# Kernel tuning notes

Hardware: AMD Instinct MI355X
Metric: run time of the kernel (lower is better)

## Reference

```python
import jax, jax.numpy as jnp
import numpy as np

W_SCALE = 0.05  # keep gates out of hard saturation


def _lstm_dir(x_tbd, Wih, Whh, b, reverse):
    """One direction of one LSTM layer. x_tbd: [T,B,Din]. Returns hs [T,B,H]."""
    H = Whh.shape[1]
    B = x_tbd.shape[1]
    # precompute input projections for all timesteps: [T,B,4H]
    xp = jnp.einsum('tbd,gd->tbg', x_tbd, Wih) + b
    if reverse:
        xp = xp[::-1]

    def step(carry, xg):
        h, c = carry
        gates = xg + h @ Whh.T  # [B,4H], PyTorch gate order i,f,g,o
        i, f, g, o = jnp.split(gates, 4, axis=-1)
        i = jax.nn.sigmoid(i)
        f = jax.nn.sigmoid(f)
        g = jnp.tanh(g)
        o = jax.nn.sigmoid(o)
        c = f * c + i * g
        h = o * jnp.tanh(c)
        return (h, c), h

    h0 = jnp.zeros((B, H), dtype=x_tbd.dtype)
    c0 = jnp.zeros((B, H), dtype=x_tbd.dtype)
    _, hs = jax.lax.scan(step, (h0, c0), xp)
    if reverse:
        hs = hs[::-1]
    return hs


def setup_inputs() -> dict:
    key = jax.random.key(0)
    ks = jax.random.split(key, 8)
    B, T, V, E, H, L = 32, 512, 32000, 1024, 512, 2
    inp = jax.random.randint(ks[0], (B, T), 0, V)
    emb = jax.random.normal(ks[1], (V, E), dtype=jnp.float32) * W_SCALE
    Wih = jax.random.normal(ks[2], (L, 2, 4 * H, E), dtype=jnp.float32) * W_SCALE
    Whh = jax.random.normal(ks[3], (L, 2, 4 * H, H), dtype=jnp.float32) * W_SCALE
    bih = jax.random.normal(ks[4], (L, 2, 4 * H), dtype=jnp.float32) * W_SCALE
    bhh = jax.random.normal(ks[5], (L, 2, 4 * H), dtype=jnp.float32) * W_SCALE
    Wout = jax.random.normal(ks[6], (1, 2 * H), dtype=jnp.float32) * W_SCALE
    bout = jax.random.normal(ks[7], (1,), dtype=jnp.float32) * W_SCALE
    return {"inp": inp, "emb": emb, "Wih": Wih, "Whh": Whh,
            "bih": bih, "bhh": bhh, "Wout": Wout, "bout": bout}


def reference(inp, emb, Wih, Whh, bih, bhh, Wout, bout):
    H = Whh.shape[-1]
    L = Wih.shape[0]
    x = emb[inp]                      # [B,T,E] embedding lookup
    x = jnp.transpose(x, (1, 0, 2))   # [T,B,E] time-major for scan
    for l in range(L):
        b_f = bih[l, 0] + bhh[l, 0]
        b_r = bih[l, 1] + bhh[l, 1]
        h_f = _lstm_dir(x, Wih[l, 0], Whh[l, 0], b_f, reverse=False)
        h_r = _lstm_dir(x, Wih[l, 1], Whh[l, 1], b_r, reverse=True)
        x = jnp.concatenate([h_f, h_r], axis=-1)  # [T,B,2H]
        # dropout between layers is identity in eval mode
    vec = jnp.transpose(x, (1, 0, 2))  # [B,T,2H]
    nor_out = vec[:, -1, :H]           # last step of forward direction
    rev_out = vec[:, 0, H:]            # first step of reverse direction
    pooled = jnp.concatenate([nor_out, rev_out], axis=1)  # [B,2H]
    out = pooled @ Wout.T + bout       # [B,1]
    return jnp.squeeze(out, axis=-1)   # [B]
```

## Files before the change

kernel.cpp:

```cpp
#include <hip/hip_runtime.h>
#include <stdint.h>

typedef unsigned short u16;
typedef unsigned int u32;
typedef __attribute__((ext_vector_type(8))) short short8;
typedef __attribute__((ext_vector_type(4))) float f32x4;

#define T_SEQ 512
#define NB 32
#define EMBD 1024
#define HID 512
#define G4 2048
#define NROWS (T_SEQ * NB)
#define XPW 4096
#define WPD 32

static __device__ __forceinline__ u16 f2bf(float x) {
  unsigned u = __float_as_uint(x);
  u += 0x7fffu + ((u >> 16) & 1u);
  return (u16)(u >> 16);
}
static __device__ __forceinline__ float bf2f(u16 b) {
  return __uint_as_float(((unsigned)b) << 16);
}
static __device__ __forceinline__ f32x4 mfma16(short8 a, short8 b, f32x4 c) {
  return __builtin_amdgcn_mfma_f32_16x16x32_bf16(a, b, c, 0, 0, 0);
}
static __device__ __forceinline__ float fast_tanh(float x) {
  float e = __expf(2.f * x);
  return 1.f - 2.f / (e + 1.f);
}
static __device__ __forceinline__ float sigm(float x) {
  return 1.f / (1.f + __expf(-x));
}

__global__ void k_prep(const float* __restrict__ Wih, const float* __restrict__ Whh,
                       const float* __restrict__ bih, const float* __restrict__ bhh,
                       u16* __restrict__ wih_b, u16* __restrict__ whh_hi,
                       u16* __restrict__ whh_lo, float* __restrict__ bcat) {
  size_t stride = (size_t)gridDim.x * blockDim.x;
  size_t i0 = (size_t)blockIdx.x * blockDim.x + threadIdx.x;
  const size_t n_ih = (size_t)2 * 2 * G4 * EMBD;
  for (size_t i = i0; i < n_ih; i += stride) wih_b[i] = f2bf(Wih[i]);
  const size_t n_hh = (size_t)2 * 2 * G4 * HID;
  for (size_t i = i0; i < n_hh; i += stride) {
    float w = Whh[i];
    u16 hi = f2bf(w);
    whh_hi[i] = hi;
    whh_lo[i] = f2bf(w - bf2f(hi));
  }
  for (size_t i = i0; i < 2 * 4096; i += stride) {
    size_t l = i >> 12, col = i & 4095;
    bcat[i] = bih[l * 4096 + col] + bhh[l * 4096 + col];
  }
}

__global__ void k_gather(const int* __restrict__ inp, const float* __restrict__ emb,
                         u16* __restrict__ X) {
  int row = blockIdx.x;
  int t = row >> 5, b = row & 31;
  int tok = inp[b * T_SEQ + t];
  const float* src = emb + (size_t)tok * EMBD + threadIdx.x * 4;
  float4 v = *reinterpret_cast<const float4*>(src);
  ushort4 o;
  o.x = f2bf(v.x); o.y = f2bf(v.y); o.z = f2bf(v.z); o.w = f2bf(v.w);
  *reinterpret_cast<ushort4*>(X + (size_t)row * EMBD + threadIdx.x * 4) = o;
}

#define GBM 128
#define GBN 128
#define GBK 64
__global__ __launch_bounds__(256) void k_gemm(const u16* __restrict__ A,
                                              const u16* __restrict__ B,
                                              const float* __restrict__ bias,
                                              u16* __restrict__ C) {
  __shared__ u16 As[GBM][GBK];
  __shared__ u16 Bs[GBN][GBK];
  const int Kdim = 1024, Ndim = 4096;
  int bm = blockIdx.x, bn = blockIdx.y;
  int tid = threadIdx.x;
  int lane = tid & 63, wave = tid >> 6;
  int wm = wave >> 1, wn = wave & 1;
  int l15 = lane & 15, klo = (lane >> 4) * 8;
  f32x4 acc[4][4] = {};
  for (int k0 = 0; k0 < Kdim; k0 += GBK) {
#pragma unroll
    for (int s = 0; s < 4; s++) {
      int seg = tid + s * 256;
      int r = seg >> 3, cs = (seg & 7) * 8;
      *reinterpret_cast<short8*>(&As[r][cs]) =
          *reinterpret_cast<const short8*>(A + (size_t)(bm * GBM + r) * Kdim + k0 + cs);
      *reinterpret_cast<short8*>(&Bs[r][cs]) =
          *reinterpret_cast<const short8*>(B + (size_t)(bn * GBN + r) * Kdim + k0 + cs);
    }
    __syncthreads();
#pragma unroll
    for (int kk = 0; kk < GBK; kk += 32) {
      short8 af[4], bfb[4];
#pragma unroll
      for (int i = 0; i < 4; i++)
        af[i] = *reinterpret_cast<const short8*>(&As[wm * 64 + i * 16 + l15][kk + klo]);
#pragma unroll
      for (int j = 0; j < 4; j++)
        bfb[j] = *reinterpret_cast<const short8*>(&Bs[wn * 64 + j * 16 + l15][kk + klo]);
#pragma unroll
      for (int i = 0; i < 4; i++)
#pragma unroll
        for (int j = 0; j < 4; j++)
          acc[i][j] = mfma16(af[i], bfb[j], acc[i][j]);
    }
    __syncthreads();
  }
  int lg4 = (lane >> 4) * 4;
#pragma unroll
  for (int i = 0; i < 4; i++) {
#pragma unroll
    for (int j = 0; j < 4; j++) {
      int n = bn * GBN + wn * 64 + j * 16 + l15;
      float bv = bias[n];
#pragma unroll
      for (int r = 0; r < 4; r++) {
        int m = bm * GBM + wm * 64 + i * 16 + lg4 + r;
        C[(size_t)m * Ndim + n] = f2bf(acc[i][j][r] + bv);
      }
    }
  }
}

__global__ __launch_bounds__(256, 1) void k_lstm7(const u16* __restrict__ xp,
                                                  const u16* __restrict__ whh_hi,
                                                  const u16* __restrict__ whh_lo,
                                                  u32* __restrict__ ypk,
                                                  u16* __restrict__ yh,
                                                  int* __restrict__ flags,
                                                  int write_yh) {
  int blk = blockIdx.x;
  int dir = blk >> 5, slice = blk & 31;
  int tid = threadIdx.x, wave = tid >> 6, lane = tid & 63;
  int u0 = slice * 16;
  int l15 = lane & 15, lg = lane >> 4;
  int klo = lg * 8;

  f32x4 whf[4][4], wlf[4][4];
#pragma unroll
  for (int ct = 0; ct < 4; ct++) {
    size_t wr = ((size_t)dir * G4 + ct * HID + u0 + l15) * HID + wave * 128 + klo;
#pragma unroll
    for (int kt = 0; kt < 4; kt++) {
      whf[ct][kt] = *reinterpret_cast<const f32x4*>(whh_hi + wr + kt * 32);
      wlf[ct][kt] = *reinterpret_cast<const f32x4*>(whh_lo + wr + kt * 32);
    }
  }
#pragma unroll
  for (int ct = 0; ct < 4; ct++)
#pragma unroll
    for (int kt = 0; kt < 4; kt++) {
      asm volatile("" : "+v"(whf[ct][kt]));
      asm volatile("" : "+v"(wlf[ct][kt]));
    }

  __shared__ float pgx[4][NB][16][5];
  float cst[2] = {0.f, 0.f};
  int* myflags = flags + dir * T_SEQ * WPD;
  int bj[2], uj[2];
#pragma unroll
  for (int j = 0; j < 2; j++) {
    int p = tid + 256 * j;
    uj[j] = p & 15;
    bj[j] = p >> 4;
  }

  float xq[2][4];
  auto ldxq = [&](int row) {
#pragma unroll
    for (int j = 0; j < 2; j++) {
      const u16* xb = xp + (size_t)(row * NB + bj[j]) * XPW + dir * 2048 + u0 + uj[j];
#pragma unroll
      for (int g = 0; g < 4; g++) xq[j][g] = bf2f(xb[g * HID]);
    }
    asm volatile("s_waitcnt vmcnt(0)" ::: "memory");
  };
  ldxq(dir ? (T_SEQ - 1) : 0);

  for (int s = 0; s < T_SEQ; s++) {
    int trow = dir ? (T_SEQ - 1 - s) : s;
    if (s > 0) {
      int* slot = myflags + (s - 1) * WPD + wave * 8 + (lane & 7);
      int v;
      do {
        v = __hip_atomic_load(slot, __ATOMIC_RELAXED, __HIP_MEMORY_SCOPE_AGENT);
        if (__all(v != 0)) break;
        __builtin_amdgcn_s_sleep(1);
      } while (1);
      __builtin_amdgcn_fence(__ATOMIC_ACQUIRE, "workgroup");
      int prow = dir ? (T_SEQ - s) : (s - 1);
      const u32* yb = ypk + ((size_t)prow * NB + l15) * 1024 + dir * HID + wave * 128 + klo;
      short8 ah[2][4], al[2][4];
#pragma unroll
      for (int mt = 0; mt < 2; mt++) {
        const u32* yr = yb + (size_t)mt * 16 * 1024;
#pragma unroll
        for (int kt = 0; kt < 4; kt++) {
          const uint4* p = reinterpret_cast<const uint4*>(yr + kt * 32);
          uint4 a = p[0], b = p[1];
          u32 v8[8] = {a.x, a.y, a.z, a.w, b.x, b.y, b.z, b.w};
          union { short8 s8; u32 u[4]; } uh, ul;
#pragma unroll
          for (int i = 0; i < 4; i++) {
            uh.u[i] = __builtin_amdgcn_perm(v8[2 * i + 1], v8[2 * i], 0x07060302u);
            ul.u[i] = __builtin_amdgcn_perm(v8[2 * i + 1], v8[2 * i], 0x05040100u);
          }
          ah[mt][kt] = uh.s8;
          al[mt][kt] = ul.s8;
        }
      }
      f32x4 accM[2][4], accC[2][4];
#pragma unroll
      for (int mt = 0; mt < 2; mt++)
#pragma unroll
        for (int ct = 0; ct < 4; ct++) {
          accM[mt][ct] = (f32x4){0.f, 0.f, 0.f, 0.f};
          accC[mt][ct] = (f32x4){0.f, 0.f, 0.f, 0.f};
        }
#pragma unroll
      for (int kt = 0; kt < 4; kt++)
#pragma unroll
        for (int mt = 0; mt < 2; mt++)
#pragma unroll
          for (int ct = 0; ct < 4; ct++) {
            short8 wh = __builtin_bit_cast(short8, whf[ct][kt]);
            short8 wl = __builtin_bit_cast(short8, wlf[ct][kt]);
            accM[mt][ct] = mfma16(ah[mt][kt], wh, accM[mt][ct]);
            accC[mt][ct] = mfma16(al[mt][kt], wh, accC[mt][ct]);
            accC[mt][ct] = mfma16(ah[mt][kt], wl, accC[mt][ct]);
          }
#pragma unroll
      for (int mt = 0; mt < 2; mt++)
#pragma unroll
        for (int ct = 0; ct < 4; ct++) {
          f32x4 v4 = accM[mt][ct] + accC[mt][ct];
#pragma unroll
          for (int r = 0; r < 4; r++)
            pgx[ct][mt * 16 + lg * 4 + r][l15][wave] = v4[r];
        }
    }
    __syncthreads();
#pragma unroll
    for (int j = 0; j < 2; j++) {
      int b = bj[j], uu = uj[j];
      float gs[4];
#pragma unroll
      for (int g = 0; g < 4; g++) {
        float v = xq[j][g];
        if (s > 0)
          v += (pgx[g][b][uu][0] + pgx[g][b][uu][1]) +
               (pgx[g][b][uu][2] + pgx[g][b][uu][3]);
        gs[g] = v;
      }
      float iv = sigm(gs[0]);
      float fv = sigm(gs[1]);
      float gv = fast_tanh(gs[2]);
      float ov = sigm(gs[3]);
      float c = fv * cst[j] + iv * gv;
      cst[j] = c;
      float h = ov * fast_tanh(c);
      u16 hh = f2bf(h);
      u16 hl = f2bf(h - bf2f(hh));
      size_t yo = ((size_t)trow * NB + b) * 1024 + dir * HID + u0 + uu;
      __hip_atomic_store(ypk + yo, ((u32)hh << 16) | hl, __ATOMIC_RELAXED,
                         __HIP_MEMORY_SCOPE_AGENT);
      if (write_yh) yh[yo] = hh;
    }
    __syncthreads();
    if (tid == 0)
      __hip_atomic_store(myflags + s * WPD + slice, 1, __ATOMIC_RELAXED,
                         __HIP_MEMORY_SCOPE_AGENT);
    if (s + 1 < T_SEQ)
      ldxq(dir ? (T_SEQ - 2 - s) : (s + 1));
  }
}

__global__ void k_out(const u32* __restrict__ ypk, const float* __restrict__ wout,
                      const float* __restrict__ bout, float* __restrict__ out) {
  int b = blockIdx.x;
  __shared__ float red[256];
  float s = 0.f;
  for (int c = threadIdx.x; c < 1024; c += 256) {
    size_t row = (c < 512) ? ((size_t)(T_SEQ - 1) * NB + b) : (size_t)b;
    u32 pk = ypk[row * 1024 + c];
    float h = bf2f((u16)(pk >> 16)) + bf2f((u16)(pk & 0xFFFFu));
    s += h * wout[c];
  }
  red[threadIdx.x] = s;
  __syncthreads();
  for (int st = 128; st > 0; st >>= 1) {
    if (threadIdx.x < st) red[threadIdx.x] += red[threadIdx.x + st];
    __syncthreads();
  }
  if (threadIdx.x == 0) out[b] = red[0] + bout[0];
}

extern "C" void kernel_launch(void* const* d_in, const int* in_sizes, int n_in,
                              void* d_out, int out_size, void* d_ws, size_t ws_size,
                              hipStream_t stream) {
  const int*   inp  = (const int*)d_in[0];
  const float* emb  = (const float*)d_in[1];
  const float* Wih  = (const float*)d_in[2];
  const float* Whh  = (const float*)d_in[3];
  const float* bih  = (const float*)d_in[4];
  const float* bhh  = (const float*)d_in[5];
  const float* Wout = (const float*)d_in[6];
  const float* bout = (const float*)d_in[7];
  float* out = (float*)d_out;
  char* ws = (char*)d_ws;

  const size_t SZ_XP  = (size_t)NROWS * XPW * 2;
  const size_t SZ_YPK = (size_t)NROWS * 1024 * 4;
  const size_t SZ_YH  = (size_t)NROWS * 1024 * 2;
  const size_t SZ_WIH = (size_t)2 * 4096 * 1024 * 2;
  const size_t SZ_WHH = (size_t)2 * 2 * G4 * HID * 2;
  const size_t SZ_FLG = (size_t)2 * 2 * T_SEQ * WPD * sizeof(int);
  size_t off = 0;
  auto alloc = [&](size_t n) { size_t o = off; off += (n + 255) & ~(size_t)255; return o; };
  size_t o_xp   = alloc(SZ_XP);
  size_t o_ypk  = alloc(SZ_YPK);
  size_t o_y1h  = alloc(SZ_YH);
  size_t o_x1   = alloc(SZ_YH);
  size_t o_wih  = alloc(SZ_WIH);
  size_t o_whhh = alloc(SZ_WHH);
  size_t o_whhl = alloc(SZ_WHH);
  size_t o_bc   = alloc(2 * 4096 * sizeof(float));
  size_t o_flg  = alloc(SZ_FLG);
  if (ws_size < off) return;

  u16* xp   = (u16*)(ws + o_xp);
  u32* ypk  = (u32*)(ws + o_ypk);
  u16* y1h  = (u16*)(ws + o_y1h);
  u16* x1   = (u16*)(ws + o_x1);
  u16* wihb = (u16*)(ws + o_wih);
  u16* whhh = (u16*)(ws + o_whhh);
  u16* whhl = (u16*)(ws + o_whhl);
  float* bc = (float*)(ws + o_bc);
  int* flg  = (int*)(ws + o_flg);

  hipMemsetAsync(flg, 0, SZ_FLG, stream);
  k_prep<<<4096, 256, 0, stream>>>(Wih, Whh, bih, bhh, wihb, whhh, whhl, bc);
  k_gather<<<NROWS, 256, 0, stream>>>(inp, emb, x1);
  k_gemm<<<dim3(NROWS / GBM, XPW / GBN), 256, 0, stream>>>(x1, wihb, bc, xp);
  k_lstm7<<<2 * WPD, 256, 0, stream>>>(xp, whhh, whhl, ypk, y1h, flg, 1);
  k_gemm<<<dim3(NROWS / GBM, XPW / GBN), 256, 0, stream>>>(
      y1h, wihb + (size_t)4096 * 1024, bc + 4096, xp);
  k_lstm7<<<2 * WPD, 256, 0, stream>>>(xp, whhh + (size_t)2 * G4 * HID,
                                       whhl + (size_t)2 * G4 * HID, ypk, y1h,
                                       flg + 2 * T_SEQ * WPD, 0);
  k_out<<<NB, 256, 0, stream>>>(ypk, Wout, bout, out);
}
```

Before: 5.464 ms.

## Replace flag-based inter-block sync with sentinel polling on the hidden-state buffer

Removes the separate per-step flag array. Blocks now poll the packed hidden-state rows directly with cache-bypassing loads until no word equals the 0xFFFFFFFF sentinel. The output buffers are pre-filled with the sentinel by memset, and the second layer's buffer reuses the dead y1h/x1 workspace. This removes the extra barrier, flag store and flag-load round trip on every recurrent step. The next step's input-projection loads are also issued while the MFMA work runs rather than after the flag store. The costs are two extra 64MB memsets and heavier polling traffic, since each poll reloads the full hidden tile.

```diff
diff --git a/kernel.cpp b/kernel.cpp
--- a/kernel.cpp
+++ b/kernel.cpp
@@ -14,6 +14,7 @@
 #define NROWS (T_SEQ * NB)
 #define XPW 4096
 #define WPD 32
+#define SENTW 0xFFFFFFFFu
 
 static __device__ __forceinline__ u16 f2bf(float x) {
   unsigned u = __float_as_uint(x);
@@ -32,6 +33,11 @@
 }
 static __device__ __forceinline__ float sigm(float x) {
   return 1.f / (1.f + __expf(-x));
+}
+static __device__ __forceinline__ void barrier_lds() {
+  asm volatile("s_waitcnt lgkmcnt(0)" ::: "memory");
+  __builtin_amdgcn_s_barrier();
+  asm volatile("" ::: "memory");
 }
 
 __global__ void k_prep(const float* __restrict__ Wih, const float* __restrict__ Whh,
@@ -127,12 +133,11 @@
   }
 }
 
-__global__ __launch_bounds__(256, 1) void k_lstm7(const u16* __restrict__ xp,
+__global__ __launch_bounds__(256, 1) void k_lstm8(const u16* __restrict__ xp,
                                                   const u16* __restrict__ whh_hi,
                                                   const u16* __restrict__ whh_lo,
                                                   u32* __restrict__ ypk,
                                                   u16* __restrict__ yh,
-                                                  int* __restrict__ flags,
                                                   int write_yh) {
   int blk = blockIdx.x;
   int dir = blk >> 5, slice = blk & 31;
@@ -161,7 +166,6 @@
 
   __shared__ float pgx[4][NB][16][5];
   float cst[2] = {0.f, 0.f};
-  int* myflags = flags + dir * T_SEQ * WPD;
   int bj[2], uj[2];
 #pragma unroll
   for (int j = 0; j < 2; j++) {
@@ -170,39 +174,44 @@
     bj[j] = p >> 4;
   }
 
-  float xq[2][4];
-  auto ldxq = [&](int row) {
-#pragma unroll
-    for (int j = 0; j < 2; j++) {
-      const u16* xb = xp + (size_t)(row * NB + bj[j]) * XPW + dir * 2048 + u0 + uj[j];
-#pragma unroll
-      for (int g = 0; g < 4; g++) xq[j][g] = bf2f(xb[g * HID]);
-    }
-    asm volatile("s_waitcnt vmcnt(0)" ::: "memory");
-  };
-  ldxq(dir ? (T_SEQ - 1) : 0);
-
   for (int s = 0; s < T_SEQ; s++) {
     int trow = dir ? (T_SEQ - 1 - s) : s;
+    short8 ah[2][4], al[2][4];
     if (s > 0) {
-      int* slot = myflags + (s - 1) * WPD + wave * 8 + (lane & 7);
-      int v;
-      do {
-        v = __hip_atomic_load(slot, __ATOMIC_RELAXED, __HIP_MEMORY_SCOPE_AGENT);
-        if (__all(v != 0)) break;
-        __builtin_amdgcn_s_sleep(1);
-      } while (1);
-      __builtin_amdgcn_fence(__ATOMIC_ACQUIRE, "workgroup");
       int prow = dir ? (T_SEQ - s) : (s - 1);
       const u32* yb = ypk + ((size_t)prow * NB + l15) * 1024 + dir * HID + wave * 128 + klo;
-      short8 ah[2][4], al[2][4];
-#pragma unroll
-      for (int mt = 0; mt < 2; mt++) {
-        const u32* yr = yb + (size_t)mt * 16 * 1024;
+      uint4 hb[2][4][2];
+      while (true) {
+#pragma unroll
+        for (int mt = 0; mt < 2; mt++) {
+          const u32* pb = yb + (size_t)mt * 16 * 1024;
+#pragma unroll
+          for (int kt = 0; kt < 4; kt++) {
+            asm volatile("global_load_dwordx4 %0, %1, off offset:%2 sc0 sc1"
+                         : "=&v"(hb[mt][kt][0]) : "v"(pb), "i"(kt * 128));
+            asm volatile("global_load_dwordx4 %0, %1, off offset:%2 sc0 sc1"
+                         : "=&v"(hb[mt][kt][1]) : "v"(pb), "i"(kt * 128 + 16));
+          }
+        }
+        asm volatile("s_waitcnt vmcnt(0)" ::: "memory");
+        __builtin_amdgcn_sched_barrier(0);
+        u32 mx = 0;
+#pragma unroll
+        for (int mt = 0; mt < 2; mt++)
+#pragma unroll
+          for (int kt = 0; kt < 4; kt++)
+#pragma unroll
+            for (int h2 = 0; h2 < 2; h2++) {
+              uint4 v = hb[mt][kt][h2];
+              mx = max(mx, max(max(v.x, v.y), max(v.z, v.w)));
+            }
+        if (__all(mx != SENTW)) break;
+      }
+#pragma unroll
+      for (int mt = 0; mt < 2; mt++)
 #pragma unroll
         for (int kt = 0; kt < 4; kt++) {
-          const uint4* p = reinterpret_cast<const uint4*>(yr + kt * 32);
-          uint4 a = p[0], b = p[1];
+          uint4 a = hb[mt][kt][0], b = hb[mt][kt][1];
           u32 v8[8] = {a.x, a.y, a.z, a.w, b.x, b.y, b.z, b.w};
           union { short8 s8; u32 u[4]; } uh, ul;
 #pragma unroll
@@ -213,7 +222,17 @@
           ah[mt][kt] = uh.s8;
           al[mt][kt] = ul.s8;
         }
-      }
+    }
+    u32 xqr[2][4];
+#pragma unroll
+    for (int j = 0; j < 2; j++) {
+      const u16* xb = xp + (size_t)(trow * NB + bj[j]) * XPW + dir * 2048 + u0 + uj[j];
+#pragma unroll
+      for (int g = 0; g < 4; g++)
+        asm volatile("global_load_ushort %0, %1, off offset:%2"
+                     : "=&v"(xqr[j][g]) : "v"(xb), "i"(g * HID * 2));
+    }
+    if (s > 0) {
       f32x4 accM[2][4], accC[2][4];
 #pragma unroll
       for (int mt = 0; mt < 2; mt++)
@@ -244,14 +263,16 @@
             pgx[ct][mt * 16 + lg * 4 + r][l15][wave] = v4[r];
         }
     }
-    __syncthreads();
+    barrier_lds();
+    asm volatile("s_waitcnt vmcnt(0)" ::: "memory");
+    __builtin_amdgcn_sched_barrier(0);
 #pragma unroll
     for (int j = 0; j < 2; j++) {
       int b = bj[j], uu = uj[j];
       float gs[4];
 #pragma unroll
       for (int g = 0; g < 4; g++) {
-        float v = xq[j][g];
+        float v = bf2f((u16)xqr[j][g]);
         if (s > 0)
           v += (pgx[g][b][uu][0] + pgx[g][b][uu][1]) +
                (pgx[g][b][uu][2] + pgx[g][b][uu][3]);
@@ -271,12 +292,7 @@
                          __HIP_MEMORY_SCOPE_AGENT);
       if (write_yh) yh[yo] = hh;
     }
-    __syncthreads();
-    if (tid == 0)
-      __hip_atomic_store(myflags + s * WPD + slice, 1, __ATOMIC_RELAXED,
-                         __HIP_MEMORY_SCOPE_AGENT);
-    if (s + 1 < T_SEQ)
-      ldxq(dir ? (T_SEQ - 2 - s) : (s + 1));
+    barrier_lds();
   }
 }
 
@@ -319,39 +335,37 @@
   const size_t SZ_YH  = (size_t)NROWS * 1024 * 2;
   const size_t SZ_WIH = (size_t)2 * 4096 * 1024 * 2;
   const size_t SZ_WHH = (size_t)2 * 2 * G4 * HID * 2;
-  const size_t SZ_FLG = (size_t)2 * 2 * T_SEQ * WPD * sizeof(int);
   size_t off = 0;
   auto alloc = [&](size_t n) { size_t o = off; off += (n + 255) & ~(size_t)255; return o; };
   size_t o_xp   = alloc(SZ_XP);
-  size_t o_ypk  = alloc(SZ_YPK);
+  size_t o_ypkA = alloc(SZ_YPK);
   size_t o_y1h  = alloc(SZ_YH);
   size_t o_x1   = alloc(SZ_YH);
   size_t o_wih  = alloc(SZ_WIH);
   size_t o_whhh = alloc(SZ_WHH);
   size_t o_whhl = alloc(SZ_WHH);
   size_t o_bc   = alloc(2 * 4096 * sizeof(float));
-  size_t o_flg  = alloc(SZ_FLG);
   if (ws_size < off) return;
 
   u16* xp   = (u16*)(ws + o_xp);
-  u32* ypk  = (u32*)(ws + o_ypk);
+  u32* ypkA = (u32*)(ws + o_ypkA);
   u16* y1h  = (u16*)(ws + o_y1h);
   u16* x1   = (u16*)(ws + o_x1);
+  u32* ypkB = (u32*)(ws + o_y1h);
   u16* wihb = (u16*)(ws + o_wih);
   u16* whhh = (u16*)(ws + o_whhh);
   u16* whhl = (u16*)(ws + o_whhl);
   float* bc = (float*)(ws + o_bc);
-  int* flg  = (int*)(ws + o_flg);
-
-  hipMemsetAsync(flg, 0, SZ_FLG, stream);
+
+  hipMemsetAsync(ypkA, 0xFF, SZ_YPK, stream);
   k_prep<<<4096, 256, 0, stream>>>(Wih, Whh, bih, bhh, wihb, whhh, whhl, bc);
   k_gather<<<NROWS, 256, 0, stream>>>(inp, emb, x1);
   k_gemm<<<dim3(NROWS / GBM, XPW / GBN), 256, 0, stream>>>(x1, wihb, bc, xp);
-  k_lstm7<<<2 * WPD, 256, 0, stream>>>(xp, whhh, whhl, ypk, y1h, flg, 1);
+  k_lstm8<<<2 * WPD, 256, 0, stream>>>(xp, whhh, whhl, ypkA, y1h, 1);
   k_gemm<<<dim3(NROWS / GBM, XPW / GBN), 256, 0, stream>>>(
       y1h, wihb + (size_t)4096 * 1024, bc + 4096, xp);
-  k_lstm7<<<2 * WPD, 256, 0, stream>>>(xp, whhh + (size_t)2 * G4 * HID,
-                                       whhl + (size_t)2 * G4 * HID, ypk, y1h,
-                                       flg + 2 * T_SEQ * WPD, 0);
-  k_out<<<NB, 256, 0, stream>>>(ypk, Wout, bout, out);
-}
+  hipMemsetAsync(ypkB, 0xFF, SZ_YPK, stream);
+  k_lstm8<<<2 * WPD, 256, 0, stream>>>(xp, whhh + (size_t)2 * G4 * HID,
+                                       whhl + (size_t)2 * G4 * HID, ypkB, y1h, 0);
+  k_out<<<NB, 256, 0, stream>>>(ypkB, Wout, bout, out);
+}
```

Measured after the change: 5.380 ms. No clear change (-1.5%).
